# Optimization experiments

Hardware: AMD Instinct MI355X
Metric: run time of the kernel (lower is better)

The kernel has to match this reference:

```python
import jax, jax.numpy as jnp
import numpy as np

EPS = 1e-7  # keras.backend.epsilon()
ROUTINGS = 3
N_IN, D_IN = 2048, 16
CAPS_N, CAPS_DIM = 64, 32
BATCH = 32


def squash(x, axis=-1):
    s2 = jnp.sum(jnp.square(x), axis=axis, keepdims=True) + EPS
    return (jnp.sqrt(s2) / (1.0 + s2)) * x


def setup_inputs() -> dict:
    key = jax.random.key(0)
    kx, kw = jax.random.split(key)
    x = jax.random.normal(kx, (BATCH, N_IN, D_IN), dtype=jnp.float32)
    # glorot_uniform for W: fan_in = caps_dim_in, fan_out = caps_dim_out (per matmul tile)
    limit = np.sqrt(6.0 / (D_IN + CAPS_DIM))
    W = jax.random.uniform(kw, (N_IN, CAPS_N, CAPS_DIM, D_IN), minval=-limit, maxval=limit, dtype=jnp.float32)
    return {"x": x, "W": W}


def reference(x, W):
    # caps_predicted (u_hat): W[i,k] @ x[b,i] -> [B, n_in, caps_n, caps_dim]
    u_hat = jnp.einsum('ikdl,bil->bikd', W, x)
    # routing logits, broadcast over batch like the original [1, n_in, caps_n, 1, 1]
    b = jnp.zeros((1, N_IN, CAPS_N), dtype=x.dtype)
    v = None
    for r in range(ROUTINGS):
        c = jax.nn.softmax(b, axis=2)                      # [*, n_in, caps_n]
        s = jnp.sum(c[..., None] * u_hat, axis=1)          # [B, caps_n, caps_dim]
        v = squash(s, axis=-1)                             # [B, caps_n, caps_dim]
        if r < ROUTINGS - 1:
            # agreement = u_hat^T . v  -> [B, n_in, caps_n]
            agreement = jnp.einsum('bikd,bkd->bik', u_hat, v)
            b = b + agreement
    return v
```

## Files before the change

### kernel.cpp

```cpp
#include <hip/hip_runtime.h>
#include <hip/hip_fp16.h>

#define BB 32
#define NI 2048
#define NK 64
#define ND 32
#define KD 2048
#define NL 16
#define NCH0 64
#define NRC 32
#define EPSF 1e-7f

typedef _Float16 f16;
typedef _Float16 h2 __attribute__((ext_vector_type(2)));
typedef __attribute__((ext_vector_type(4))) float f32x4;
union U4H8 { uint4 u4; h2 h[4]; };
union U2H4 { uint2 u2; h2 h[2]; };

static __device__ __forceinline__ float dot2f(h2 a, h2 b, float c) {
#if __has_builtin(__builtin_amdgcn_fdot2)
  return __builtin_amdgcn_fdot2(a, b, c, false);
#else
  return c + (float)a[0] * (float)b[0] + (float)a[1] * (float)b[1];
#endif
}

static __device__ __forceinline__ float fastrcp(float s) {
#if __has_builtin(__builtin_amdgcn_rcpf)
  return __builtin_amdgcn_rcpf(s);
#else
  return 1.0f / s;
#endif
}

static __device__ __forceinline__ h2 pack2(float x, float y) {
  h2 r; r[0] = (_Float16)x; r[1] = (_Float16)y; return r;
}

__global__ __launch_bounds__(512, 2) void k_uhat(const float* __restrict__ x,
                                                 const float* __restrict__ W,
                                                 __half* __restrict__ uhat) {
  const int i = blockIdx.x;
  const int t = threadIdx.x;
  __shared__ float xs[BB * NL];
  {
    const int b = t >> 4, l = t & 15;
    xs[t] = x[((size_t)b * NI + i) * NL + l];
  }
  __syncthreads();
  float w[4][NL];
  const float* Wp = W + (size_t)i * KD * NL + (size_t)t * 4 * NL;
  #pragma unroll
  for (int c = 0; c < 4; ++c)
    #pragma unroll
    for (int q = 0; q < 4; ++q)
      *(float4*)&w[c][q * 4] = *(const float4*)(Wp + c * NL + q * 4);
  __half* up = uhat + (size_t)i * KD + (size_t)t * 4;
  for (int b = 0; b < BB; ++b) {
    float a0 = 0.f, a1 = 0.f, a2 = 0.f, a3 = 0.f;
    #pragma unroll
    for (int l = 0; l < NL; ++l) {
      const float xv = xs[b * NL + l];
      a0 += w[0][l] * xv; a1 += w[1][l] * xv;
      a2 += w[2][l] * xv; a3 += w[3][l] * xv;
    }
    U2H4 o;
    o.h[0] = pack2(a0, a1);
    o.h[1] = pack2(a2, a3);
    *(uint2*)(up + (size_t)b * NI * KD) = o.u2;
  }
}

__global__ __launch_bounds__(256) void k_round0(const __half* __restrict__ uhat,
                                                __half* __restrict__ part) {
  const int ch = blockIdx.x, b = blockIdx.y, t = threadIdx.x;
  float acc[8];
  #pragma unroll
  for (int j = 0; j < 8; ++j) acc[j] = 0.f;
  const __half* up = uhat + ((size_t)b * NI + (size_t)ch * 32) * KD + t * 8;
  for (int il = 0; il < 32; ++il) {
    U4H8 u; u.u4 = *(const uint4*)(up + (size_t)il * KD);
    #pragma unroll
    for (int j = 0; j < 4; ++j) {
      acc[2 * j]     += (float)u.h[j][0];
      acc[2 * j + 1] += (float)u.h[j][1];
    }
  }
  U4H8 o;
  #pragma unroll
  for (int j = 0; j < 4; ++j)
    o.h[j] = pack2(acc[2 * j] * (1.f / 64.f), acc[2 * j + 1] * (1.f / 64.f));
  *(uint4*)&part[((size_t)b * NCH0 + ch) * KD + t * 8] = o.u4;
}

__global__ __launch_bounds__(256) void k_route(const __half* __restrict__ uhat,
                                               const float* __restrict__ vin,
                                               __half* __restrict__ part) {
  const int ch = blockIdx.x, b = blockIdx.y, t = threadIdx.x;
  const int wv = t >> 6, lane = t & 63;

  h2 vh[16];
  #pragma unroll
  for (int q = 0; q < 8; ++q) {
    const f32x4 v = *(const f32x4*)&vin[(size_t)b * KD + lane * ND + 4 * q];
    vh[2 * q]     = pack2(v[0], v[1]);
    vh[2 * q + 1] = pack2(v[2], v[3]);
  }

  float sacc[32];
  #pragma unroll
  for (int d = 0; d < 32; ++d) sacc[d] = 0.f;

  const __half* ub = uhat + (size_t)b * NI * KD + lane * ND;
  const int i00 = ch * 64 + wv;
  U4H8 curA[4], curB[4];
  #pragma unroll
  for (int q = 0; q < 4; ++q) {
    curA[q].u4 = *(const uint4*)(ub + (size_t)i00 * KD + 8 * q);
    curB[q].u4 = *(const uint4*)(ub + (size_t)(i00 + 4) * KD + 8 * q);
  }

  for (int p = 0; p < 8; ++p) {
    U4H8 nxtA[4], nxtB[4];
    if (p + 1 < 8) {
      const size_t oA = (size_t)(i00 + 8 * (p + 1)) * KD;
      #pragma unroll
      for (int q = 0; q < 4; ++q) {
        nxtA[q].u4 = *(const uint4*)(ub + oA + 8 * q);
        nxtB[q].u4 = *(const uint4*)(ub + oA + 4 * KD + 8 * q);
      }
    }
    float agA = 0.f, agB = 0.f;
    #pragma unroll
    for (int q = 0; q < 4; ++q)
      #pragma unroll
      for (int j = 0; j < 4; ++j) {
        agA = dot2f(curA[q].h[j], vh[4 * q + j], agA);
        agB = dot2f(curB[q].h[j], vh[4 * q + j], agB);
      }
    const float eA = __expf(agA);
    const float eB = __expf(agB);
    float sA = eA, sB = eB;
    sA += __shfl_xor(sA, 1);  sB += __shfl_xor(sB, 1);
    sA += __shfl_xor(sA, 2);  sB += __shfl_xor(sB, 2);
    sA += __shfl_xor(sA, 4);  sB += __shfl_xor(sB, 4);
    sA += __shfl_xor(sA, 8);  sB += __shfl_xor(sB, 8);
    sA += __shfl_xor(sA, 16); sB += __shfl_xor(sB, 16);
    sA += __shfl_xor(sA, 32); sB += __shfl_xor(sB, 32);
    const float cA = eA * fastrcp(sA);
    const float cB = eB * fastrcp(sB);
    #pragma unroll
    for (int q = 0; q < 4; ++q)
      #pragma unroll
      for (int j = 0; j < 4; ++j) {
        sacc[8 * q + 2 * j]     += cA * (float)curA[q].h[j][0]
                                 + cB * (float)curB[q].h[j][0];
        sacc[8 * q + 2 * j + 1] += cA * (float)curA[q].h[j][1]
                                 + cB * (float)curB[q].h[j][1];
      }
    #pragma unroll
    for (int q = 0; q < 4; ++q) { curA[q] = nxtA[q]; curB[q] = nxtB[q]; }
  }

  __shared__ float red[4][ND][64];
  #pragma unroll
  for (int d = 0; d < ND; ++d) red[wv][d][lane] = sacc[d];
  __syncthreads();
  const int k = t >> 2, d0 = (t & 3) * 8;
  float s[8];
  #pragma unroll
  for (int j = 0; j < 8; ++j)
    s[j] = red[0][d0 + j][k] + red[1][d0 + j][k] +
           red[2][d0 + j][k] + red[3][d0 + j][k];
  U4H8 o;
  #pragma unroll
  for (int j = 0; j < 4; ++j)
    o.h[j] = pack2(s[2 * j], s[2 * j + 1]);
  *(uint4*)&part[((size_t)b * NRC + ch) * KD + 8 * t] = o.u4;
}

__global__ __launch_bounds__(256) void k_reduce(const __half* __restrict__ part,
                                                int nch,
                                                const float* __restrict__ vprev,
                                                float* __restrict__ vout) {
  const int g = blockIdx.x, b = blockIdx.y, t = threadIdx.x;
  const int p = g * 256 + t;
  const h2* pp = (const h2*)part;
  const size_t base = (size_t)b * nch * (KD / 2) + p;
  float s0 = 0.f, s1 = 0.f;
  for (int ch = 0; ch < nch; ++ch) {
    const h2 v = pp[base + (size_t)ch * (KD / 2)];
    s0 += (float)v[0]; s1 += (float)v[1];
  }
  float sq = s0 * s0 + s1 * s1;
  sq += __shfl_xor(sq, 1); sq += __shfl_xor(sq, 2);
  sq += __shfl_xor(sq, 4); sq += __shfl_xor(sq, 8);
  sq += EPSF;
  const float sc = sqrtf(sq) / (1.f + sq);
  float r0 = s0 * sc, r1 = s1 * sc;
  if (vprev != nullptr) {
    r0 += vprev[(size_t)b * KD + 2 * p];
    r1 += vprev[(size_t)b * KD + 2 * p + 1];
  }
  *(float2*)&vout[(size_t)b * KD + 2 * p] = make_float2(r0, r1);
}

extern "C" void kernel_launch(void* const* d_in, const int* in_sizes, int n_in,
                              void* d_out, int out_size, void* d_ws, size_t ws_size,
                              hipStream_t stream) {
  const float* x = (const float*)d_in[0];
  const float* W = (const float*)d_in[1];
  float* out = (float*)d_out;
  char* ws = (char*)d_ws;
  __half* uhat  = (__half*)ws;
  __half* part0 = (__half*)(ws + 268435456ull);
  __half* partR = (__half*)(ws + 268435456ull + 8388608ull);
  float*  vA    = (float*)(ws + 268435456ull + 8388608ull + 4194304ull);
  float*  vB    = vA + (size_t)BB * KD;

  k_uhat<<<NI, 512, 0, stream>>>(x, W, uhat);
  k_round0<<<dim3(NCH0, BB), 256, 0, stream>>>(uhat, part0);
  k_reduce<<<dim3(4, BB), 256, 0, stream>>>(part0, NCH0, nullptr, vA);
  k_route<<<dim3(NRC, BB), 256, 0, stream>>>(uhat, vA, partR);
  k_reduce<<<dim3(4, BB), 256, 0, stream>>>(partR, NRC, vA, vB);
  k_route<<<dim3(NRC, BB), 256, 0, stream>>>(uhat, vB, partR);
  k_reduce<<<dim3(4, BB), 256, 0, stream>>>(partR, NRC, nullptr, out);
}
```

Before: 289.5 us.

## Fuse u_hat computation with round-0 partial sums into one kernel

Merges the u_hat projection kernel and the round-0 summation kernel, so each thread accumulates per-batch sums over 8 input capsules while writing u_hat. This removes a full re-read of the 256MB fp16 u_hat tensor for routing round 0. In exchange the work split changes: each thread now handles one output element across 32 batches with scalar 2-byte stores and scalar x loads, and the partial buffer grows to 256 chunks, which makes the following reduce longer.

```diff
diff --git a/kernel.cpp b/kernel.cpp
--- a/kernel.cpp
+++ b/kernel.cpp
@@ -7,7 +7,8 @@
 #define ND 32
 #define KD 2048
 #define NL 16
-#define NCH0 64
+#define ITC 8
+#define NTC (NI/ITC)
 #define NRC 32
 #define EPSF 1e-7f
 
@@ -15,7 +16,6 @@
 typedef _Float16 h2 __attribute__((ext_vector_type(2)));
 typedef __attribute__((ext_vector_type(4))) float f32x4;
 union U4H8 { uint4 u4; h2 h[4]; };
-union U2H4 { uint2 u2; h2 h[2]; };
 
 static __device__ __forceinline__ float dot2f(h2 a, h2 b, float c) {
 #if __has_builtin(__builtin_amdgcn_fdot2)
@@ -37,60 +37,40 @@
   h2 r; r[0] = (_Float16)x; r[1] = (_Float16)y; return r;
 }
 
-__global__ __launch_bounds__(512, 2) void k_uhat(const float* __restrict__ x,
+__global__ __launch_bounds__(512, 4) void k_conv(const float* __restrict__ x,
                                                  const float* __restrict__ W,
-                                                 __half* __restrict__ uhat) {
-  const int i = blockIdx.x;
-  const int t = threadIdx.x;
-  __shared__ float xs[BB * NL];
-  {
-    const int b = t >> 4, l = t & 15;
-    xs[t] = x[((size_t)b * NI + i) * NL + l];
-  }
-  __syncthreads();
-  float w[4][NL];
-  const float* Wp = W + (size_t)i * KD * NL + (size_t)t * 4 * NL;
-  #pragma unroll
-  for (int c = 0; c < 4; ++c)
+                                                 __half* __restrict__ uhat,
+                                                 __half* __restrict__ part) {
+  const int blk = blockIdx.x, quad = blockIdx.y, t = threadIdx.x;
+  const int i0 = blk * ITC;
+  const int c0 = quad * 512 + t;
+
+  float sacc[BB];
+  #pragma unroll
+  for (int b = 0; b < BB; ++b) sacc[b] = 0.f;
+
+  for (int ii = 0; ii < ITC; ++ii) {
+    const int i = i0 + ii;
+    float w[NL];
+    const float* Wp = W + ((size_t)i * KD + c0) * NL;
     #pragma unroll
     for (int q = 0; q < 4; ++q)
-      *(float4*)&w[c][q * 4] = *(const float4*)(Wp + c * NL + q * 4);
-  __half* up = uhat + (size_t)i * KD + (size_t)t * 4;
-  for (int b = 0; b < BB; ++b) {
-    float a0 = 0.f, a1 = 0.f, a2 = 0.f, a3 = 0.f;
-    #pragma unroll
-    for (int l = 0; l < NL; ++l) {
-      const float xv = xs[b * NL + l];
-      a0 += w[0][l] * xv; a1 += w[1][l] * xv;
-      a2 += w[2][l] * xv; a3 += w[3][l] * xv;
+      *(float4*)&w[4 * q] = *(const float4*)(Wp + 4 * q);
+    const float* xp = x + (size_t)i * NL;
+    __half* up = uhat + (size_t)i * KD + c0;
+    #pragma unroll
+    for (int b = 0; b < BB; ++b) {
+      const float* xb = xp + (size_t)b * NI * NL;
+      float u = 0.f;
+      #pragma unroll
+      for (int l = 0; l < NL; ++l) u += w[l] * xb[l];
+      up[(size_t)b * NI * KD] = (__half)u;
+      sacc[b] += u;
     }
-    U2H4 o;
-    o.h[0] = pack2(a0, a1);
-    o.h[1] = pack2(a2, a3);
-    *(uint2*)(up + (size_t)b * NI * KD) = o.u2;
-  }
-}
-
-__global__ __launch_bounds__(256) void k_round0(const __half* __restrict__ uhat,
-                                                __half* __restrict__ part) {
-  const int ch = blockIdx.x, b = blockIdx.y, t = threadIdx.x;
-  float acc[8];
-  #pragma unroll
-  for (int j = 0; j < 8; ++j) acc[j] = 0.f;
-  const __half* up = uhat + ((size_t)b * NI + (size_t)ch * 32) * KD + t * 8;
-  for (int il = 0; il < 32; ++il) {
-    U4H8 u; u.u4 = *(const uint4*)(up + (size_t)il * KD);
-    #pragma unroll
-    for (int j = 0; j < 4; ++j) {
-      acc[2 * j]     += (float)u.h[j][0];
-      acc[2 * j + 1] += (float)u.h[j][1];
-    }
-  }
-  U4H8 o;
-  #pragma unroll
-  for (int j = 0; j < 4; ++j)
-    o.h[j] = pack2(acc[2 * j] * (1.f / 64.f), acc[2 * j + 1] * (1.f / 64.f));
-  *(uint4*)&part[((size_t)b * NCH0 + ch) * KD + t * 8] = o.u4;
+  }
+  #pragma unroll
+  for (int b = 0; b < BB; ++b)
+    part[((size_t)b * NTC + blk) * KD + c0] = (__half)(sacc[b] * (1.f / 64.f));
 }
 
 __global__ __launch_bounds__(256) void k_route(const __half* __restrict__ uhat,
@@ -214,13 +194,12 @@
   char* ws = (char*)d_ws;
   __half* uhat  = (__half*)ws;
   __half* part0 = (__half*)(ws + 268435456ull);
-  __half* partR = (__half*)(ws + 268435456ull + 8388608ull);
-  float*  vA    = (float*)(ws + 268435456ull + 8388608ull + 4194304ull);
+  __half* partR = (__half*)(ws + 268435456ull + 33554432ull);
+  float*  vA    = (float*)(ws + 268435456ull + 33554432ull + 4194304ull);
   float*  vB    = vA + (size_t)BB * KD;
 
-  k_uhat<<<NI, 512, 0, stream>>>(x, W, uhat);
-  k_round0<<<dim3(NCH0, BB), 256, 0, stream>>>(uhat, part0);
-  k_reduce<<<dim3(4, BB), 256, 0, stream>>>(part0, NCH0, nullptr, vA);
+  k_conv<<<dim3(NTC, 4), 512, 0, stream>>>(x, W, uhat, part0);
+  k_reduce<<<dim3(4, BB), 256, 0, stream>>>(part0, NTC, nullptr, vA);
   k_route<<<dim3(NRC, BB), 256, 0, stream>>>(uhat, vA, partR);
   k_reduce<<<dim3(4, BB), 256, 0, stream>>>(partR, NRC, vA, vB);
   k_route<<<dim3(NRC, BB), 256, 0, stream>>>(uhat, vB, partR);
```

Measured after the change: 837.1 us. +189.2%, slower.
